# Performance work log

Hardware: AMD Instinct MI355X
Metric: run time of the kernel (lower is better)

## Reference

```python
import jax, jax.numpy as jnp
import numpy as np
from jax import lax

CIN, COUT, K, PAD = 256, 128, 3, 1


def setup_inputs() -> dict:
    key = jax.random.key(0)
    ks = jax.random.split(key, 5)
    N, h0, w0 = 2, 64, 64
    x = jax.random.normal(ks[0], (N, CIN, h0, w0), jnp.float32)
    lateral_feat = jax.random.normal(ks[1], (N, COUT, 1, 1), jnp.float32)
    trans_w = jax.random.normal(ks[2], (CIN, COUT, K, K), jnp.float32) * 0.02
    off_w1 = jax.random.normal(ks[3], (64, COUT, 3, 3), jnp.float32) * 0.02
    off_b1 = jnp.zeros((64,), jnp.float32)
    off_w2 = jax.random.normal(ks[4], (2 * K * K, 64, 3, 3), jnp.float32) * 0.02
    off_b2 = jnp.zeros((2 * K * K,), jnp.float32)
    return dict(x=x, lateral_feat=lateral_feat, trans_w=trans_w,
                off_w1=off_w1, off_b1=off_b1, off_w2=off_w2, off_b2=off_b2)


def _conv2d(x, w, b, pad):
    y = lax.conv_general_dilated(x, w, (1, 1), [(pad, pad), (pad, pad)],
                                 dimension_numbers=('NCHW', 'OIHW', 'NCHW'))
    return y + b[None, :, None, None]


def _conv_transpose2d(x, w, stride, pad, out_pad):
    # torch ConvTranspose2d weight layout: [Cin, Cout, k, k]
    k = w.shape[2]
    wt = jnp.flip(w, (2, 3)).transpose(1, 0, 2, 3)  # [Cout, Cin, k, k]
    lo = k - 1 - pad
    hi = k - 1 - pad + out_pad
    return lax.conv_general_dilated(x, wt, (1, 1), [(lo, hi), (lo, hi)],
                                    lhs_dilation=(stride, stride),
                                    dimension_numbers=('NCHW', 'OIHW', 'NCHW'))


def _deform_conv2d(x, offset, w, pad):
    # x [N,C,H,W], offset [N,2*K*K,H,W] (y,x interleaved per kernel tap), w [O,C,K,K]
    N, C, H, W = x.shape
    O = w.shape[0]
    KK = K * K
    off = offset.reshape(N, KK, 2, H, W)
    ky = jnp.arange(KK) // K
    kx = jnp.arange(KK) % K
    py = jnp.arange(H)[None, None, :, None] + (ky - pad)[None, :, None, None] + off[:, :, 0]
    px = jnp.arange(W)[None, None, None, :] + (kx - pad)[None, :, None, None] + off[:, :, 1]
    y0 = jnp.floor(py)
    x0 = jnp.floor(px)
    dy = py - y0
    dx = px - x0
    y0i = y0.astype(jnp.int32)
    x0i = x0.astype(jnp.int32)
    xf = x.reshape(N, C, H * W)

    def corner(yi, xi, wgt):
        valid = (yi >= 0) & (yi < H) & (xi >= 0) & (xi < W)
        idx = (jnp.clip(yi, 0, H - 1) * W + jnp.clip(xi, 0, W - 1)).reshape(N, -1)
        v = jnp.take_along_axis(xf, idx[:, None, :], axis=2).reshape(N, C, KK, H, W)
        return v * (wgt * valid)[:, None]

    sampled = (corner(y0i, x0i, (1 - dy) * (1 - dx))
               + corner(y0i, x0i + 1, (1 - dy) * dx)
               + corner(y0i + 1, x0i, dy * (1 - dx))
               + corner(y0i + 1, x0i + 1, dy * dx))  # [N,C,KK,H,W]
    return jnp.einsum('nckhw,ock->nohw', sampled, w.reshape(O, C, KK))


def reference(x, lateral_feat, trans_w, off_w1, off_b1, off_w2, off_b2):
    up = _conv_transpose2d(x, trans_w, 2, PAD, 1)          # [N, COUT, 2h0, 2w0]
    h = jax.nn.relu(_conv2d(lateral_feat, off_w1, off_b1, 1))
    offset = jnp.tanh(_conv2d(h, off_w2, off_b2, 1))       # [N, 18, 1, 1]
    N, C, H, W = up.shape
    # offset.repeat(1, 1, H, W) with 1x1 spatial input == broadcast to full grid
    offset = jnp.broadcast_to(offset, (N, 2 * K * K, H, W))
    # deform_conv2d uses trans_conv weight [O=CIN, I=COUT, K, K], stride=1, pad=PAD
    return _deform_conv2d(up, offset, trans_w, PAD)        # [N, CIN, H, W]
```

## Files before the change

### kernel.cpp

```cpp
#include <hip/hip_runtime.h>
#include <hip/hip_bf16.h>
#include <math.h>

typedef __attribute__((ext_vector_type(8))) short s16x8;
typedef __attribute__((ext_vector_type(4))) float f32x4;
typedef __attribute__((ext_vector_type(2))) float v2f;

__device__ __forceinline__ unsigned short f2bf(float f) {
    union { float f; unsigned int u; } v; v.f = f;
    unsigned int u = v.u + 0x7FFFu + ((v.u >> 16) & 1u);
    return (unsigned short)(u >> 16);
}
__device__ __forceinline__ unsigned pk2(float lo, float hi) {
    __hip_bfloat162 h = __float22bfloat162_rn(make_float2(lo, hi));
    union { __hip_bfloat162 h; unsigned u; } v; v.h = h;
    return v.u;
}
__device__ __forceinline__ v2f up2(unsigned u) {
    union { unsigned u; float f; } a, b;
    a.u = u << 16; b.u = u & 0xffff0000u;
    v2f r; r.x = a.f; r.y = b.f; return r;
}

__device__ __forceinline__ void blend4(uint4 uA, uint4 uB, uint4 uC, uint4 uD,
                                       float4 cw, unsigned short* dst) {
    v2f c00 = (v2f){cw.x, cw.x}, c01 = (v2f){cw.y, cw.y};
    v2f c10 = (v2f){cw.z, cw.z}, c11 = (v2f){cw.w, cw.w};
    unsigned ua[4] = {uA.x, uA.y, uA.z, uA.w};
    unsigned ub[4] = {uB.x, uB.y, uB.z, uB.w};
    unsigned uc[4] = {uC.x, uC.y, uC.z, uC.w};
    unsigned ud[4] = {uD.x, uD.y, uD.z, uD.w};
    unsigned pk[4];
#pragma unroll
    for (int i = 0; i < 4; ++i) {
        v2f r = c00 * up2(ua[i]) + c01 * up2(ub[i]) + c10 * up2(uc[i]) + c11 * up2(ud[i]);
        pk[i] = pk2(r.x, r.y);
    }
    *(uint4*)dst = make_uint4(pk[0], pk[1], pk[2], pk[3]);
}

__global__ __launch_bounds__(256) void k_prep(const float* __restrict__ x,
                                              const float* __restrict__ lat,
                                              const float* __restrict__ tw,
                                              const float* __restrict__ w1,
                                              const float* __restrict__ b1,
                                              const float* __restrict__ w2,
                                              const float* __restrict__ b2,
                                              unsigned short* __restrict__ xp,
                                              unsigned short* __restrict__ A2f,
                                              unsigned short* __restrict__ Awf,
                                              int* __restrict__ ipar,
                                              float* __restrict__ fpar) {
    __shared__ float sm[8420];
    int b = blockIdx.x, t = threadIdx.x;
    if (b == 0) {
        for (int i = t; i < 8192; i += 256) sm[(i >> 7) * 129 + (i & 127)] = w1[i * 9 + 4];
        __syncthreads();
        if (t < 128) {
            int n = t >> 6, o = t & 63;
            float s = b1[o];
            const float* ln = lat + n * 128;
#pragma unroll 8
            for (int c = 0; c < 128; ++c) s += ln[c] * sm[o * 129 + c];
            sm[8256 + t] = fmaxf(s, 0.f);
        }
        __syncthreads();
        if (t < 36) {
            int n = t / 18, j = t % 18;
            float s = b2[j];
            for (int o = 0; o < 64; ++o) s += sm[8256 + n * 64 + o] * w2[(j * 64 + o) * 9 + 4];
            float ov = tanhf(s);
            ov = fminf(fmaxf(ov, -0.999999f), 0.999999f);
            sm[8384 + t] = ov;
        }
        __syncthreads();
        if (t < 36) {
            int n = t / 18, j = t % 18;
            int tap = j >> 1, d = j & 1;
            float ov = sm[8384 + t];
            float fl = floorf(ov);
            int kc = d ? (tap % 3) : (tap / 3);
            ipar[(n * 9 + tap) * 2 + d] = kc - 1 + (int)fl;
            fpar[(n * 9 + tap) * 2 + d] = ov - fl;
        }
    } else if (b < 145) {
        int slot = (b - 1) * 256 + t;
        int l = slot & 63;
        int mi = (slot >> 6) & 3;
        int w = (slot >> 8) & 3;
        int k = slot >> 10;
        int row = w * 64 + mi * 16 + (l & 15);
        int kq = l >> 4;
        unsigned short v[8];
#pragma unroll
        for (int j = 0; j < 8; ++j) {
            int kcol = k * 32 + kq * 8 + j;
            int tap = kcol >> 7, c = kcol & 127;
            v[j] = f2bf(tw[(row * 128 + c) * 9 + tap]);
        }
        unsigned p0 = (unsigned)v[0] | ((unsigned)v[1] << 16);
        unsigned p1 = (unsigned)v[2] | ((unsigned)v[3] << 16);
        unsigned p2 = (unsigned)v[4] | ((unsigned)v[5] << 16);
        unsigned p3 = (unsigned)v[6] | ((unsigned)v[7] << 16);
        *(uint4*)(A2f + slot * 8) = make_uint4(p0, p1, p2, p3);
    } else if (b < 289) {
        int slot = (b - 145) * 256 + t;
        int l = slot & 63;
        int mi = (slot >> 6) & 3;
        int wm = (slot >> 8) & 1;
        int k = slot >> 9;
        int row = wm * 64 + mi * 16 + (l & 15);
        int kq = l >> 4;
        unsigned short v[8];
#pragma unroll
        for (int j = 0; j < 8; ++j) {
            int kcol = k * 32 + kq * 8 + j;
            int t9 = kcol >> 8, ci = kcol & 255;
            int ky = t9 / 3, kx = t9 - ky * 3;
            v[j] = f2bf(tw[(ci * 128 + row) * 9 + (2 - ky) * 3 + (2 - kx)]);
        }
        unsigned p0 = (unsigned)v[0] | ((unsigned)v[1] << 16);
        unsigned p1 = (unsigned)v[2] | ((unsigned)v[3] << 16);
        unsigned p2 = (unsigned)v[4] | ((unsigned)v[5] << 16);
        unsigned p3 = (unsigned)v[6] | ((unsigned)v[7] << 16);
        *(uint4*)(Awf + slot * 8) = make_uint4(p0, p1, p2, p3);
    } else {
        int bb = b - 289;
        int h = bb & 63, cq = (bb >> 6) & 3, n = bb >> 8;
        int c0 = cq * 64;
        {
            int wcol = t & 63, sub = t >> 6;
            for (int r = 0; r < 16; ++r) {
                int ci_l = r * 4 + sub;
                sm[ci_l * 65 + wcol] = x[((n * 256 + c0 + ci_l) * 64 + h) * 64 + wcol];
            }
        }
        __syncthreads();
        int wcol = t >> 2, cg = t & 3;
        unsigned short* dst = xp + (size_t)n * (65 * 65 * 256) + (h * 65 + wcol) * 256 + c0 + cg * 16;
        unsigned pk[8];
#pragma unroll
        for (int j = 0; j < 8; ++j)
            pk[j] = pk2(sm[(cg * 16 + 2 * j) * 65 + wcol], sm[(cg * 16 + 2 * j + 1) * 65 + wcol]);
        *(uint4*)dst = make_uint4(pk[0], pk[1], pk[2], pk[3]);
        *(uint4*)(dst + 8) = make_uint4(pk[4], pk[5], pk[6], pk[7]);
    }
}

__global__ __launch_bounds__(256) void k_tconv4(const unsigned short* __restrict__ xp,
                                                const unsigned short* __restrict__ Awf,
                                                unsigned short* __restrict__ upp) {
    int t = threadIdx.x;
    int b = blockIdx.x;
    int cls = b >> 7;
    int phase = (cls < 2) ? 1 : 0;
    int xpar = 1 - (cls & 1);
    int idx = b & 127;
    int n = idx >> 6, yh = idx & 63;
    int y = 2 * yh + phase;
    const unsigned short* xpn = xp + (size_t)n * (65 * 65 * 256);

    int lane = t & 63, w = t >> 6;
    int col = lane & 15, q = lane >> 4;
    int pos = w * 16 + col;

    int nky = phase ? 2 : 1;
    int nkx = xpar ? 2 : 1;

    f32x4 acc[8];
#pragma unroll
    for (int mi = 0; mi < 8; ++mi) acc[mi] = (f32x4){0.f, 0.f, 0.f, 0.f};

    const unsigned short* Afl = Awf + lane * 8;

    for (int a1 = 0; a1 < nky; ++a1) {
        int ky = phase ? (a1 ? 2 : 0) : 1;
        int d2 = (y + ky - 1) >> 1;
        for (int a2 = 0; a2 < nkx; ++a2) {
            int kx = xpar ? (a2 ? 2 : 0) : 1;
            int s = (xpar + kx - 1) >> 1;
            int t9 = ky * 3 + kx;
            const unsigned short* bptr = xpn + ((size_t)(d2 * 65 + s + pos)) * 256 + q * 8;
            const unsigned short* aptr = Afl + t9 * 8 * 4096;
#pragma unroll 2
            for (int cb = 0; cb < 8; ++cb) {
                s16x8 bf = *(const s16x8*)(bptr + cb * 32);
                s16x8 a[8];
#pragma unroll
                for (int mi = 0; mi < 8; ++mi)
                    a[mi] = *(const s16x8*)(aptr + cb * 4096 + (mi >> 2) * 2048 + (mi & 3) * 512);
#pragma unroll
                for (int mi = 0; mi < 8; ++mi)
                    acc[mi] = __builtin_amdgcn_mfma_f32_16x16x32_bf16(a[mi], bf, acc[mi], 0, 0, 0);
            }
        }
    }

    unsigned short* uppn = upp + (size_t)n * (132 * 132 * 128);
    int xg = 2 * pos + xpar;
#pragma unroll
    for (int mi = 0; mi < 8; ++mi) {
        int co = mi * 16 + q * 4;
        unsigned short* p = uppn + ((y + 2) * 132 + (xg + 2)) * 128 + co;
        unsigned lo = pk2(acc[mi][0], acc[mi][1]);
        unsigned hi = pk2(acc[mi][2], acc[mi][3]);
        *(uint2*)p = make_uint2(lo, hi);
    }
}

__global__ __launch_bounds__(512, 4) void k_deform6(const unsigned short* __restrict__ upp,
                                                    const unsigned short* __restrict__ A2f,
                                                    const int* __restrict__ ipar,
                                                    const float* __restrict__ fpar,
                                                    float* __restrict__ out) {
    __shared__ unsigned short Bs[2][64][84];
    __shared__ int sbase[9];
    __shared__ float4 swt[9];
    int t = threadIdx.x;
    int b = blockIdx.x;
    int xcd = b & 7, j = b >> 3;
    int n = xcd >> 2, band = xcd & 3;
    int y = band * 32 + (j & 31);
    int tx0 = (j >> 5) * 64;
    const unsigned short* uppn = upp + (size_t)n * (132 * 132 * 128);

    int lane = t & 63, w = t >> 6;
    int wm = w & 3, wn = w >> 2;
    int col = lane & 15, q = lane >> 4;
    int bx = t >> 3, sub = t & 7;
    int cst = sub >> 2, bcg = sub & 3;
    int boff = bx * 128 + cst * 32 + bcg * 8;

    if (t < 9) {
        int iy = ipar[(n * 9 + t) * 2 + 0], ix = ipar[(n * 9 + t) * 2 + 1];
        float fy = fpar[(n * 9 + t) * 2 + 0], fx = fpar[(n * 9 + t) * 2 + 1];
        sbase[t] = ((y + 2 + iy) * 132 + (tx0 + 2 + ix)) * 128;
        swt[t] = make_float4((1.f - fy) * (1.f - fx), (1.f - fy) * fx, fy * (1.f - fx), fy * fx);
    }

    f32x4 acc[4][2];
#pragma unroll
    for (int mi = 0; mi < 4; ++mi)
#pragma unroll
        for (int ni = 0; ni < 2; ++ni) acc[mi][ni] = (f32x4){0.f, 0.f, 0.f, 0.f};

    __syncthreads();

    const unsigned short* Afw = A2f + wm * 2048 + lane * 8;
    s16x8 a_ev[4], a_od[4];
    uint4 cA, cB, cC, cD;
    float4 cwp;

    {
        const unsigned short* p = uppn + sbase[0] + boff;
        uint4 uA = *(const uint4*)p;
        uint4 uB = *(const uint4*)(p + 128);
        uint4 uC = *(const uint4*)(p + 16896);
        uint4 uD = *(const uint4*)(p + 17024);
        blend4(uA, uB, uC, uD, swt[0], &Bs[0][bx][cst * 42 + bcg * 8]);
        const unsigned short* p2 = p + 64;
        cA = *(const uint4*)p2;
        cB = *(const uint4*)(p2 + 128);
        cC = *(const uint4*)(p2 + 16896);
        cD = *(const uint4*)(p2 + 17024);
        cwp = swt[0];
#pragma unroll
        for (int mi = 0; mi < 4; ++mi)
            a_ev[mi] = *(const s16x8*)(Afw + mi * 512);
    }
    __syncthreads();

    for (int kk = 0; kk < 18; ++kk) {
        int cur = kk & 1;
        if (kk < 17)
            blend4(cA, cB, cC, cD, cwp, &Bs[cur ^ 1][bx][cst * 42 + bcg * 8]);
        if (kk < 16) {
            int k2 = kk + 2;
            int tap2 = k2 >> 1, cb0 = (k2 & 1) * 64;
            cwp = swt[tap2];
            const unsigned short* p = uppn + sbase[tap2] + cb0 + boff;
            cA = *(const uint4*)p;
            cB = *(const uint4*)(p + 128);
            cC = *(const uint4*)(p + 16896);
            cD = *(const uint4*)(p + 17024);
        }
        {
            int nc = 2 * kk + 1;
#pragma unroll
            for (int mi = 0; mi < 4; ++mi)
                a_od[mi] = *(const s16x8*)(Afw + nc * 8192 + mi * 512);
            s16x8 bf[2];
#pragma unroll
            for (int ni = 0; ni < 2; ++ni)
                bf[ni] = *(const s16x8*)&Bs[cur][wn * 32 + ni * 16 + col][q * 8];
#pragma unroll
            for (int mi = 0; mi < 4; ++mi)
#pragma unroll
                for (int ni = 0; ni < 2; ++ni)
                    acc[mi][ni] = __builtin_amdgcn_mfma_f32_16x16x32_bf16(a_ev[mi], bf[ni], acc[mi][ni], 0, 0, 0);
        }
        {
            if (kk < 17) {
                int nc = 2 * (kk + 1);
#pragma unroll
                for (int mi = 0; mi < 4; ++mi)
                    a_ev[mi] = *(const s16x8*)(Afw + nc * 8192 + mi * 512);
            }
            s16x8 bf[2];
#pragma unroll
            for (int ni = 0; ni < 2; ++ni)
                bf[ni] = *(const s16x8*)&Bs[cur][wn * 32 + ni * 16 + col][42 + q * 8];
#pragma unroll
            for (int mi = 0; mi < 4; ++mi)
#pragma unroll
                for (int ni = 0; ni < 2; ++ni)
                    acc[mi][ni] = __builtin_amdgcn_mfma_f32_16x16x32_bf16(a_od[mi], bf[ni], acc[mi][ni], 0, 0, 0);
        }
        __syncthreads();
    }

#pragma unroll
    for (int mi = 0; mi < 4; ++mi)
#pragma unroll
        for (int ni = 0; ni < 2; ++ni) {
            int o = wm * 64 + mi * 16 + q * 4;
            int xg = tx0 + wn * 32 + ni * 16 + col;
            float* p = out + (((size_t)(n * 256 + o)) * 128 + y) * 128 + xg;
            p[0]         = acc[mi][ni][0];
            p[16384]     = acc[mi][ni][1];
            p[2 * 16384] = acc[mi][ni][2];
            p[3 * 16384] = acc[mi][ni][3];
        }
}

extern "C" void kernel_launch(void* const* d_in, const int* in_sizes, int n_in,
                              void* d_out, int out_size, void* d_ws, size_t ws_size,
                              hipStream_t stream) {
    const float* x   = (const float*)d_in[0];
    const float* lat = (const float*)d_in[1];
    const float* tw  = (const float*)d_in[2];
    const float* w1  = (const float*)d_in[3];
    const float* b1  = (const float*)d_in[4];
    const float* w2  = (const float*)d_in[5];
    const float* b2  = (const float*)d_in[6];
    float* out = (float*)d_out;

    char* ws = (char*)d_ws;
    unsigned short* upp = (unsigned short*)ws;
    unsigned short* xp  = (unsigned short*)(ws + 8921088);
    unsigned short* A2f = (unsigned short*)(ws + 13247488);
    unsigned short* Awf = (unsigned short*)(ws + 13837312);
    int*   ipar         = (int*)(ws + 14427136);
    float* fpar         = (float*)(ws + 14427424);

    hipMemsetAsync(ws, 0, 13247488, stream);
    k_prep<<<801, 256, 0, stream>>>(x, lat, tw, w1, b1, w2, b2, xp, A2f, Awf, ipar, fpar);
    k_tconv4<<<512, 256, 0, stream>>>(xp, Awf, upp);
    k_deform6<<<512, 512, 0, stream>>>(upp, A2f, ipar, fpar, out);
}
```

Before: 160.3 us.

## Replace full workspace memset with border-only zeroing and reshape deform pipeline

Drops the 13 MB workspace memset and adds extra blocks in the prep and transposed-conv kernels that zero only the padding halos of the padded input and upsampled buffers. The deform kernel's software pipeline is also restructured. It now prefetches one stage ahead instead of two, issues the corner loads before the MFMAs and blends after them, and rotates A-fragment registers through a cur/next pair. This removes a large memset pass and a launch, and may change register pressure and latency hiding in the deform loop. Correctness depends on every non-halo element being written by the compute kernels.

Result: no change. 157.3 us (-1.8%).

```diff
diff --git a/kernel.cpp b/kernel.cpp
--- a/kernel.cpp
+++ b/kernel.cpp
@@ -124,7 +124,7 @@
         unsigned p2 = (unsigned)v[4] | ((unsigned)v[5] << 16);
         unsigned p3 = (unsigned)v[6] | ((unsigned)v[7] << 16);
         *(uint4*)(Awf + slot * 8) = make_uint4(p0, p1, p2, p3);
-    } else {
+    } else if (b < 801) {
         int bb = b - 289;
         int h = bb & 63, cq = (bb >> 6) & 3, n = bb >> 8;
         int c0 = cq * 64;
@@ -144,6 +144,16 @@
             pk[j] = pk2(sm[(cg * 16 + 2 * j) * 65 + wcol], sm[(cg * 16 + 2 * j + 1) * 65 + wcol]);
         *(uint4*)dst = make_uint4(pk[0], pk[1], pk[2], pk[3]);
         *(uint4*)(dst + 8) = make_uint4(pk[4], pk[5], pk[6], pk[7]);
+    } else {
+        int n = b - 801;
+        unsigned short* xpn = xp + (size_t)n * (65 * 65 * 256);
+        uint4 z = make_uint4(0u, 0u, 0u, 0u);
+        for (int i = t; i < 129 * 16; i += 256) {
+            int pos = i >> 4, seg = i & 15;
+            int h, wv;
+            if (pos < 65) { h = 64; wv = pos; } else { h = pos - 65; wv = 64; }
+            *(uint4*)(xpn + (h * 65 + wv) * 256 + seg * 16) = z;
+        }
     }
 }
 
@@ -152,6 +162,22 @@
                                                 unsigned short* __restrict__ upp) {
     int t = threadIdx.x;
     int b = blockIdx.x;
+    if (b >= 512) {
+        int hb = b - 512;
+        int n = hb >> 1, half = hb & 1;
+        unsigned short* uppn = upp + (size_t)n * (132 * 132 * 128);
+        uint4 z = make_uint4(0u, 0u, 0u, 0u);
+        const int rows4[4] = {0, 1, 130, 131};
+        for (int i = t; i < 8320; i += 256) {
+            int u = half * 8320 + i;
+            int pos = u >> 4, seg = u & 15;
+            int y, xx;
+            if (pos < 528) { y = rows4[pos / 132]; xx = pos % 132; }
+            else { int j = pos - 528; y = 2 + (j >> 2); xx = rows4[j & 3] ; }
+            *(uint4*)(uppn + (y * 132 + xx) * 128 + seg * 8) = z;
+        }
+        return;
+    }
     int cls = b >> 7;
     int phase = (cls < 2) ? 1 : 0;
     int xpar = 1 - (cls & 1);
@@ -208,7 +234,7 @@
     }
 }
 
-__global__ __launch_bounds__(512, 4) void k_deform6(const unsigned short* __restrict__ upp,
+__global__ __launch_bounds__(512, 4) void k_deform7(const unsigned short* __restrict__ upp,
                                                     const unsigned short* __restrict__ A2f,
                                                     const int* __restrict__ ipar,
                                                     const float* __restrict__ fpar,
@@ -247,7 +273,7 @@
     __syncthreads();
 
     const unsigned short* Afw = A2f + wm * 2048 + lane * 8;
-    s16x8 a_ev[4], a_od[4];
+    s16x8 a_cur[4], a_nxt[4];
     uint4 cA, cB, cC, cD;
     float4 cwp;
 
@@ -257,38 +283,29 @@
         uint4 uB = *(const uint4*)(p + 128);
         uint4 uC = *(const uint4*)(p + 16896);
         uint4 uD = *(const uint4*)(p + 17024);
+#pragma unroll
+        for (int mi = 0; mi < 4; ++mi)
+            a_cur[mi] = *(const s16x8*)(Afw + mi * 512);
         blend4(uA, uB, uC, uD, swt[0], &Bs[0][bx][cst * 42 + bcg * 8]);
-        const unsigned short* p2 = p + 64;
-        cA = *(const uint4*)p2;
-        cB = *(const uint4*)(p2 + 128);
-        cC = *(const uint4*)(p2 + 16896);
-        cD = *(const uint4*)(p2 + 17024);
-        cwp = swt[0];
-#pragma unroll
-        for (int mi = 0; mi < 4; ++mi)
-            a_ev[mi] = *(const s16x8*)(Afw + mi * 512);
     }
     __syncthreads();
 
     for (int kk = 0; kk < 18; ++kk) {
         int cur = kk & 1;
-        if (kk < 17)
-            blend4(cA, cB, cC, cD, cwp, &Bs[cur ^ 1][bx][cst * 42 + bcg * 8]);
-        if (kk < 16) {
-            int k2 = kk + 2;
-            int tap2 = k2 >> 1, cb0 = (k2 & 1) * 64;
-            cwp = swt[tap2];
-            const unsigned short* p = uppn + sbase[tap2] + cb0 + boff;
+        if (kk < 17) {
+            int k1 = kk + 1;
+            int tap1 = k1 >> 1, cb0 = (k1 & 1) * 64;
+            cwp = swt[tap1];
+            const unsigned short* p = uppn + sbase[tap1] + cb0 + boff;
             cA = *(const uint4*)p;
             cB = *(const uint4*)(p + 128);
             cC = *(const uint4*)(p + 16896);
             cD = *(const uint4*)(p + 17024);
         }
         {
-            int nc = 2 * kk + 1;
 #pragma unroll
             for (int mi = 0; mi < 4; ++mi)
-                a_od[mi] = *(const s16x8*)(Afw + nc * 8192 + mi * 512);
+                a_nxt[mi] = *(const s16x8*)(Afw + (2 * kk + 1) * 8192 + mi * 512);
             s16x8 bf[2];
 #pragma unroll
             for (int ni = 0; ni < 2; ++ni)
@@ -297,14 +314,15 @@
             for (int mi = 0; mi < 4; ++mi)
 #pragma unroll
                 for (int ni = 0; ni < 2; ++ni)
-                    acc[mi][ni] = __builtin_amdgcn_mfma_f32_16x16x32_bf16(a_ev[mi], bf[ni], acc[mi][ni], 0, 0, 0);
+                    acc[mi][ni] = __builtin_amdgcn_mfma_f32_16x16x32_bf16(a_cur[mi], bf[ni], acc[mi][ni], 0, 0, 0);
+#pragma unroll
+            for (int mi = 0; mi < 4; ++mi) a_cur[mi] = a_nxt[mi];
         }
         {
             if (kk < 17) {
-                int nc = 2 * (kk + 1);
 #pragma unroll
                 for (int mi = 0; mi < 4; ++mi)
-                    a_ev[mi] = *(const s16x8*)(Afw + nc * 8192 + mi * 512);
+                    a_nxt[mi] = *(const s16x8*)(Afw + (2 * kk + 2) * 8192 + mi * 512);
             }
             s16x8 bf[2];
 #pragma unroll
@@ -314,8 +332,12 @@
             for (int mi = 0; mi < 4; ++mi)
 #pragma unroll
                 for (int ni = 0; ni < 2; ++ni)
-                    acc[mi][ni] = __builtin_amdgcn_mfma_f32_16x16x32_bf16(a_od[mi], bf[ni], acc[mi][ni], 0, 0, 0);
-        }
+                    acc[mi][ni] = __builtin_amdgcn_mfma_f32_16x16x32_bf16(a_cur[mi], bf[ni], acc[mi][ni], 0, 0, 0);
+#pragma unroll
+            for (int mi = 0; mi < 4; ++mi) a_cur[mi] = a_nxt[mi];
+        }
+        if (kk < 17)
+            blend4(cA, cB, cC, cD, cwp, &Bs[cur ^ 1][bx][cst * 42 + bcg * 8]);
         __syncthreads();
     }
 
@@ -353,8 +375,7 @@
     int*   ipar         = (int*)(ws + 14427136);
     float* fpar         = (float*)(ws + 14427424);
 
-    hipMemsetAsync(ws, 0, 13247488, stream);
-    k_prep<<<801, 256, 0, stream>>>(x, lat, tw, w1, b1, w2, b2, xp, A2f, Awf, ipar, fpar);
-    k_tconv4<<<512, 256, 0, stream>>>(xp, Awf, upp);
-    k_deform6<<<512, 512, 0, stream>>>(upp, A2f, ipar, fpar, out);
-}
+    k_prep<<<803, 256, 0, stream>>>(x, lat, tw, w1, b1, w2, b2, xp, A2f, Awf, ipar, fpar);
+    k_tconv4<<<516, 256, 0, stream>>>(xp, Awf, upp);
+    k_deform7<<<512, 512, 0, stream>>>(upp, A2f, ipar, fpar, out);
+}
```
